# Kernel tuning notes

Hardware: AMD Instinct MI355X
Metric: run time of the kernel (lower is better)

The kernel has to match this reference:

```python
import jax, jax.numpy as jnp
import numpy as np

P = 7  # adaptive max-pool output size


def _cell_masks(lo, hi, size):
    """Adaptive-pool cell membership masks.

    For a crop spanning [lo, hi) of length h, PyTorch AdaptiveMaxPool2d cell i
    covers local rows [floor(i*h/P), ceil((i+1)*h/P)). Returns bool [N, P, size].
    """
    h = hi - lo  # [N]
    i = jnp.arange(P)
    start = lo[:, None] + (i[None, :] * h[:, None]) // P            # [N,P]
    end = lo[:, None] + ((i[None, :] + 1) * h[:, None] + (P - 1)) // P  # ceil
    r = jnp.arange(size)
    return (r[None, None, :] >= start[:, :, None]) & (r[None, None, :] < end[:, :, None])


def setup_inputs() -> dict:
    key = jax.random.key(0)
    kf, kw, k1, k2, k3, k4 = jax.random.split(key, 6)
    H, W, N, C = 96, 160, 128, 2
    feature = jax.random.normal(kf, (1, C, H, W), jnp.float32)
    # valid boxes [x1, y1, x2, y2] fully inside the feature map, size in [6, 48]
    x1 = jax.random.uniform(k1, (N,), minval=0.0, maxval=W - 49.0)
    y1 = jax.random.uniform(k2, (N,), minval=0.0, maxval=H - 49.0)
    bw = jax.random.uniform(k3, (N,), minval=6.0, maxval=48.0)
    bh = jax.random.uniform(k4, (N,), minval=6.0, maxval=48.0)
    boxes = jnp.stack([x1, y1, x1 + bw, y1 + bh], axis=1)
    fc_w = jax.random.normal(kw, (4, C * P * P), jnp.float32) * 0.1
    fc_b = jnp.zeros((4,), jnp.float32)
    return {"feature": feature, "boxes": boxes, "fc_w": fc_w, "fc_b": fc_b}


def reference(feature, boxes, fc_w, fc_b):
    feat = feature[0]  # [C, H, W] (batch is 1; each box crops this map)
    C, H, W = feat.shape
    bi = boxes.astype(jnp.int32)  # int() truncation of box coords, blocks grad
    row_mask = _cell_masks(bi[:, 1], bi[:, 3], H)  # [N, 7, H]
    col_mask = _cell_masks(bi[:, 0], bi[:, 2], W)  # [N, 7, W]
    neg = jnp.array(-jnp.inf, feat.dtype)
    # pool rows: [N, C, 7, W]
    pr = jnp.max(jnp.where(row_mask[:, None, :, :, None],
                           feat[None, :, None, :, :], neg), axis=3)
    # pool cols: [N, C, 7, 7]
    pooled = jnp.max(jnp.where(col_mask[:, None, None, :, :],
                               pr[:, :, :, None, :], neg), axis=4)
    flat = pooled.reshape(pooled.shape[0], -1)  # [N, C*7*7], channel-major like torch
    deltaB = jax.nn.relu(flat @ fc_w.T + fc_b)  # [N, 4]
    return deltaB + boxes
```

## Files before the change

kernel.cpp:

```cpp
#include <hip/hip_runtime.h>
#include <hip/hip_bf16.h>
#include <math.h>


#define C_ 2
#define H_ 96
#define W_ 160
#define P_ 7
#define CELLS (C_ * P_ * P_)

__global__ void __launch_bounds__(128)
roi_pool_fc_kernel(const float* __restrict__ feature,
                   const float* __restrict__ boxes,
                   const float* __restrict__ fc_w,
                   const float* __restrict__ fc_b,
                   float* __restrict__ out)
{
    const int n = blockIdx.x;
    const int t = threadIdx.x;

    __shared__ float pooled[CELLS];

    const float bx1 = boxes[n * 4 + 0];
    const float by1 = boxes[n * 4 + 1];
    const float bx2 = boxes[n * 4 + 2];
    const float by2 = boxes[n * 4 + 3];

    const int x1 = (int)bx1;
    const int y1 = (int)by1;
    const int x2 = (int)bx2;
    const int y2 = (int)by2;
    const int hh = y2 - y1;
    const int ww = x2 - x1;

    if (t < CELLS) {
        const int c   = t / (P_ * P_);
        const int rem = t % (P_ * P_);
        const int py  = rem / P_;
        const int px  = rem % P_;

        const int rs = y1 + (py * hh) / P_;
        const int re = y1 + ((py + 1) * hh + (P_ - 1)) / P_;
        const int cs = x1 + (px * ww) / P_;
        const int ce = x1 + ((px + 1) * ww + (P_ - 1)) / P_;
        const int nr = re - rs;
        const int nc = ce - cs;

        const float* __restrict__ base = feature + c * (H_ * W_) + rs * W_ + cs;

        float v[64];
        #pragma unroll
        for (int i = 0; i < 64; ++i)
            v[i] = base[(i >> 3) * W_ + (i & 7)];

        float m = -INFINITY;
        #pragma unroll
        for (int i = 0; i < 64; ++i) {
            const bool ok = ((i >> 3) < nr) & ((i & 7) < nc);
            m = fmaxf(m, ok ? v[i] : -INFINITY);
        }
        pooled[t] = m;
    }
    __syncthreads();

    if (t < 4) {
        float w[CELLS], p[CELLS];
        const float* __restrict__ wrow = fc_w + t * CELLS;
        #pragma unroll
        for (int k = 0; k < CELLS; ++k) w[k] = wrow[k];
        #pragma unroll
        for (int k = 0; k < CELLS; ++k) p[k] = pooled[k];
        float acc = fc_b[t];
        #pragma unroll
        for (int k = 0; k < CELLS; ++k)
            acc = fmaf(p[k], w[k], acc);
        const float bc = boxes[n * 4 + t];
        out[n * 4 + t] = fmaxf(acc, 0.f) + bc;
    }
}

extern "C" void kernel_launch(void* const* d_in, const int* in_sizes, int n_in,
                              void* d_out, int out_size, void* d_ws, size_t ws_size,
                              hipStream_t stream) {
    const float* feature = (const float*)d_in[0];
    const float* boxes   = (const float*)d_in[1];
    const float* fc_w    = (const float*)d_in[2];
    const float* fc_b    = (const float*)d_in[3];
    float* out = (float*)d_out;

    const int N = in_sizes[1] / 4;

    roi_pool_fc_kernel<<<N, 128, 0, stream>>>(feature, boxes, fc_w, fc_b, out);
}
```

Before: 9.605 us.

## Fuse FC into pooling threads with wave shuffle reduction, prefetch weights

Each pooling thread now loads its four FC weights up front, multiplies its pooled max by them, and the products are summed with wavefront xor-shuffles plus a tiny two-wave shared-memory combine. This replaces the serial 98-element dot product done by four threads after the barrier. The per-cell max is also reorganised as a tree reduction for more ILP, and the box is read as a single float4. Shuffle reductions add some instructions across all lanes, and summation order changes slightly.

Result: slower. 11.72 us (+22.0%).

```diff
diff --git a/kernel.cpp b/kernel.cpp
--- a/kernel.cpp
+++ b/kernel.cpp
@@ -19,20 +19,25 @@
     const int n = blockIdx.x;
     const int t = threadIdx.x;
 
-    __shared__ float pooled[CELLS];
+    __shared__ float partial[2][4];
 
-    const float bx1 = boxes[n * 4 + 0];
-    const float by1 = boxes[n * 4 + 1];
-    const float bx2 = boxes[n * 4 + 2];
-    const float by2 = boxes[n * 4 + 3];
+    float w0 = 0.f, w1 = 0.f, w2 = 0.f, w3 = 0.f;
+    if (t < CELLS) {
+        w0 = fc_w[0 * CELLS + t];
+        w1 = fc_w[1 * CELLS + t];
+        w2 = fc_w[2 * CELLS + t];
+        w3 = fc_w[3 * CELLS + t];
+    }
 
-    const int x1 = (int)bx1;
-    const int y1 = (int)by1;
-    const int x2 = (int)bx2;
-    const int y2 = (int)by2;
+    const float4 b = ((const float4*)boxes)[n];
+    const int x1 = (int)b.x;
+    const int y1 = (int)b.y;
+    const int x2 = (int)b.z;
+    const int y2 = (int)b.w;
     const int hh = y2 - y1;
     const int ww = x2 - x1;
 
+    float m = 0.f;
     if (t < CELLS) {
         const int c   = t / (P_ * P_);
         const int rem = t % (P_ * P_);
@@ -53,28 +58,38 @@
         for (int i = 0; i < 64; ++i)
             v[i] = base[(i >> 3) * W_ + (i & 7)];
 
-        float m = -INFINITY;
         #pragma unroll
         for (int i = 0; i < 64; ++i) {
             const bool ok = ((i >> 3) < nr) & ((i & 7) < nc);
-            m = fmaxf(m, ok ? v[i] : -INFINITY);
+            v[i] = ok ? v[i] : -INFINITY;
         }
-        pooled[t] = m;
+        #pragma unroll
+        for (int s = 32; s > 0; s >>= 1) {
+            #pragma unroll
+            for (int i = 0; i < s; ++i)
+                v[i] = fmaxf(v[i], v[i + s]);
+        }
+        m = v[0];
+    }
+
+    float p0 = m * w0, p1 = m * w1, p2 = m * w2, p3 = m * w3;
+    #pragma unroll
+    for (int s = 32; s > 0; s >>= 1) {
+        p0 += __shfl_xor(p0, s);
+        p1 += __shfl_xor(p1, s);
+        p2 += __shfl_xor(p2, s);
+        p3 += __shfl_xor(p3, s);
+    }
+    const int wv = t >> 6;
+    if ((t & 63) == 0) {
+        partial[wv][0] = p0; partial[wv][1] = p1;
+        partial[wv][2] = p2; partial[wv][3] = p3;
     }
     __syncthreads();
 
     if (t < 4) {
-        float w[CELLS], p[CELLS];
-        const float* __restrict__ wrow = fc_w + t * CELLS;
-        #pragma unroll
-        for (int k = 0; k < CELLS; ++k) w[k] = wrow[k];
-        #pragma unroll
-        for (int k = 0; k < CELLS; ++k) p[k] = pooled[k];
-        float acc = fc_b[t];
-        #pragma unroll
-        for (int k = 0; k < CELLS; ++k)
-            acc = fmaf(p[k], w[k], acc);
-        const float bc = boxes[n * 4 + t];
+        const float acc = partial[0][t] + partial[1][t] + fc_b[t];
+        const float bc = (t == 0) ? b.x : (t == 1) ? b.y : (t == 2) ? b.z : b.w;
         out[n * 4 + t] = fmaxf(acc, 0.f) + bc;
     }
 }
```
